# Kernel tuning notes

Measured on AMD Instinct MI355X. Metric: run time of the kernel, lower is better.

The kernel has to match this reference:

```python
import jax, jax.numpy as jnp
import numpy as np

N, E = 50000, 640000
D_IN, D_HID, D_OUT = 128, 128, 64
NEG_SLOPE = 0.2  # PyG SuperGATConv default negative_slope


def setup_inputs() -> dict:
    key = jax.random.key(0)
    ks = jax.random.split(key, 16)
    def glorot(k, shape):
        fan = sum(shape) if len(shape) > 1 else shape[0]
        return jax.random.normal(k, shape, jnp.float32) * np.sqrt(2.0 / fan)
    return {
        "x": jax.random.normal(ks[0], (N, D_IN), jnp.float32),
        "edge_index": jax.random.randint(ks[1], (2, E), 0, N, jnp.int64 if jax.config.jax_enable_x64 else jnp.int32),
        "W0": glorot(ks[2], (D_IN, D_HID)),
        "al0": glorot(ks[3], (D_HID,)),
        "ar0": glorot(ks[4], (D_HID,)),
        "b0": jnp.zeros((D_HID,), jnp.float32),
        "W1": glorot(ks[5], (D_HID, D_HID)),
        "al1": glorot(ks[6], (D_HID,)),
        "ar1": glorot(ks[7], (D_HID,)),
        "b1": jnp.zeros((D_HID,), jnp.float32),
        "W2": glorot(ks[8], (D_HID, D_OUT)),
        "al2": glorot(ks[9], (D_OUT,)),
        "ar2": glorot(ks[10], (D_OUT,)),
        "b2": jnp.zeros((D_OUT,), jnp.float32),
    }


def _supergat_layer(x, W, att_l, att_r, b, src, dst, n):
    # heads = 1, concat=False, attention_type='MX' (PyG SuperGATConv defaults)
    h = x @ W                                   # [N, C]
    hi = h[dst]                                 # target-node features x_i, [Etot, C]
    hj = h[src]                                 # source-node features x_j, [Etot, C]
    logits = jnp.sum(hi * hj, axis=-1)          # MX dot-product gate
    alpha = hj @ att_l + hi @ att_r             # GO-style scores
    alpha = alpha * jax.nn.sigmoid(logits)      # MX mixing
    alpha = jnp.where(alpha >= 0, alpha, NEG_SLOPE * alpha)  # leaky_relu
    # segment softmax over incoming edges of each target node
    amax = jax.ops.segment_max(alpha, dst, num_segments=n)
    ex = jnp.exp(alpha - amax[dst])
    denom = jax.ops.segment_sum(ex, dst, num_segments=n)
    a = ex / (denom[dst] + 1e-16)
    out = jax.ops.segment_sum(hj * a[:, None], dst, num_segments=n)
    return out + b


def reference(x, edge_index, W0, al0, ar0, b0, W1, al1, ar1, b1, W2, al2, ar2, b2):
    n = x.shape[0]
    loops = jnp.arange(n, dtype=edge_index.dtype)  # add_self_loops=True
    src = jnp.concatenate([edge_index[0], loops])
    dst = jnp.concatenate([edge_index[1], loops])
    params = [(W0, al0, ar0, b0), (W1, al1, ar1, b1), (W2, al2, ar2, b2)]
    h = x
    for (W, al, ar, b) in params:
        h = _supergat_layer(h, W, al, ar, b, src, dst, n)
        h = jax.nn.relu(h)          # dropout is identity in eval mode
    return jax.nn.log_softmax(h, axis=-1)
```

## Files before the change

### kernel.cpp

```cpp
#include <hip/hip_runtime.h>
#include <math.h>

using short8 = __attribute__((ext_vector_type(8))) short;
using f32x4 = __attribute__((ext_vector_type(4))) float;

__device__ __forceinline__ float bflo(unsigned int u) {
  union { unsigned int i; float f; } v; v.i = u << 16; return v.f;
}
__device__ __forceinline__ float bfhi(unsigned int u) {
  union { unsigned int i; float f; } v; v.i = u & 0xFFFF0000u; return v.f;
}
__device__ __forceinline__ unsigned short f2bf1(float f) {
  union { float f; unsigned int i; } v; v.f = f;
  return (unsigned short)((v.i + 0x7FFFu + ((v.i >> 16) & 1u)) >> 16);
}
__device__ __forceinline__ unsigned int f2bf_pack(float a, float b) {
  union { float f; unsigned int i; } x, y; x.f = a; y.f = b;
  unsigned int xa = x.i + 0x7FFFu + ((x.i >> 16) & 1u);
  unsigned int yb = y.i + 0x7FFFu + ((y.i >> 16) & 1u);
  return (xa >> 16) | (yb & 0xFFFF0000u);
}

__global__ void prep0_kernel(const float* __restrict__ W0, const float* __restrict__ W1,
                             const float* __restrict__ W2, unsigned short* __restrict__ Wt0,
                             unsigned short* __restrict__ Wt1, unsigned short* __restrict__ Wt2,
                             int* __restrict__ counts, int* __restrict__ dhist, int N) {
  int i = blockIdx.x * 256 + threadIdx.x;
  int gs = gridDim.x * 256;
  for (int j = i; j < N; j += gs) counts[j] = 0;
  if (i < 1024) dhist[i] = 0;
  for (int j = i; j < 128 * 128; j += gs) {
    int c = j >> 7, k = j & 127;
    Wt0[c * 136 + k] = f2bf1(W0[(size_t)k * 128 + c]);
  }
  for (int j = i; j < 128 * 128; j += gs) {
    int c = j >> 7, k = j & 127;
    Wt1[c * 136 + k] = f2bf1(W1[(size_t)k * 128 + c]);
  }
  for (int j = i; j < 64 * 128; j += gs) {
    int c = j >> 7, k = j & 127;
    Wt2[c * 136 + k] = f2bf1(W2[(size_t)k * 64 + c]);
  }
}

__global__ void histo_kernel(const int* __restrict__ ei, int E, int N,
                             int* __restrict__ counts) {
  int e = blockIdx.x * blockDim.x + threadIdx.x;
  int etot = E + N;
  if (e >= etot) return;
  int d = (e < E) ? ei[E + e] : (e - E);
  atomicAdd(&counts[d], 1);
}

__global__ void scan1_deghist_kernel(const int* __restrict__ counts, int* __restrict__ excl,
                                     int* __restrict__ bsums, int* __restrict__ dhist, int N) {
  __shared__ int sm[256];
  __shared__ int lh[1024];
  int t = threadIdx.x;
  int i = blockIdx.x * 256 + t;
  int v = (i < N) ? counts[i] : 0;
  sm[t] = v;
  __syncthreads();
#pragma unroll
  for (int off = 1; off < 256; off <<= 1) {
    int add = (t >= off) ? sm[t - off] : 0;
    __syncthreads();
    sm[t] += add;
    __syncthreads();
  }
  if (i < N) excl[i] = sm[t] - v;
  if (t == 255) bsums[blockIdx.x] = sm[255];
  for (int q = t; q < 1024; q += 256) lh[q] = 0;
  __syncthreads();
  if (i < N) {
    int key = v < 1023 ? v : 1023;
    atomicAdd(&lh[key], 1);
  }
  __syncthreads();
  for (int q = t; q < 1024; q += 256) {
    int c = lh[q];
    if (c) atomicAdd(&dhist[q], c);
  }
}

__global__ void scan2_degscan_kernel(int* __restrict__ bsums, int nb,
                                     int* __restrict__ dhist) {
  int t = threadIdx.x;
  if (blockIdx.x == 0) {
    __shared__ int sm[256];
    int v = (t < nb) ? bsums[t] : 0;
    sm[t] = v;
    __syncthreads();
#pragma unroll
    for (int off = 1; off < 256; off <<= 1) {
      int add = (t >= off) ? sm[t - off] : 0;
      __syncthreads();
      sm[t] += add;
      __syncthreads();
    }
    if (t < nb) bsums[t] = sm[t] - v;
  } else {
    __shared__ int arr[256];
    int v0 = dhist[t * 4 + 0], v1 = dhist[t * 4 + 1];
    int v2 = dhist[t * 4 + 2], v3 = dhist[t * 4 + 3];
    int s0 = v0, s1 = s0 + v1, s2 = s1 + v2, s3 = s2 + v3;
    arr[t] = s3;
    __syncthreads();
#pragma unroll
    for (int off = 1; off < 256; off <<= 1) {
      int add = (t >= off) ? arr[t - off] : 0;
      __syncthreads();
      arr[t] += add;
      __syncthreads();
    }
    int base = (t > 0) ? arr[t - 1] : 0;
    dhist[t * 4 + 0] = base;
    dhist[t * 4 + 1] = base + s0;
    dhist[t * 4 + 2] = base + s1;
    dhist[t * 4 + 3] = base + s2;
  }
}

__global__ void scan3_kernel(const int* __restrict__ excl, const int* __restrict__ bsums,
                             int* __restrict__ rowptr, int* __restrict__ cursor,
                             int N, int etot) {
  int i = blockIdx.x * 256 + threadIdx.x;
  if (i < N) {
    int v = excl[i] + bsums[i >> 8];
    rowptr[i] = v;
    cursor[i] = v;
  }
  if (i == N) rowptr[N] = etot;
}

__global__ void scatter_degscatter_kernel(const int* __restrict__ ei, int E, int N,
                                          int* __restrict__ cursor, int* __restrict__ csr_src,
                                          const int* __restrict__ rowptr,
                                          int* __restrict__ dhist, int* __restrict__ perm) {
  int t = threadIdx.x;
  int e = blockIdx.x * 256 + t;
  int etot = E + N;
  if (e < etot) {
    int s, d;
    if (e < E) { s = ei[e]; d = ei[E + e]; } else { s = e - E; d = e - E; }
    int pos = atomicAdd(&cursor[d], 1);
    csr_src[pos] = s;
  }
  if (blockIdx.x < (N + 255) / 256) {
    __shared__ int lc[1024];
    __shared__ int lb[1024];
    for (int q = t; q < 1024; q += 256) lc[q] = 0;
    __syncthreads();
    int i = blockIdx.x * 256 + t;
    int key = 0, lr = 0;
    if (i < N) {
      int d = rowptr[i + 1] - rowptr[i];
      key = d < 1023 ? d : 1023;
      lr = atomicAdd(&lc[key], 1);
    }
    __syncthreads();
    for (int q = t; q < 1024; q += 256) {
      int c = lc[q];
      if (c) lb[q] = atomicAdd(&dhist[q], c);
    }
    __syncthreads();
    if (i < N) perm[lb[key] + lr] = i;
  }
}

template <int COLS, bool AF32>
__global__ __launch_bounds__(256) void gemm_mfma(
    const void* __restrict__ Xv, const unsigned short* __restrict__ Wt,
    const float* __restrict__ al, const float* __restrict__ ar,
    unsigned short* __restrict__ H, float* __restrict__ hl,
    float* __restrict__ hr, int N) {
  constexpr int NT = COLS / 16;
  __shared__ unsigned short Ws[COLS * 136];
  const int tid = threadIdx.x;
  {
    const unsigned int* wg = (const unsigned int*)Wt;
    unsigned int* ws = (unsigned int*)Ws;
    for (int i = tid; i < COLS * 68; i += 256) ws[i] = wg[i];
  }
  __syncthreads();

  const int w = tid >> 6, l = tid & 63;
  const int l15 = l & 15, lg = l >> 4;
  const int r0 = blockIdx.x * 64 + w * 16;

  f32x4 acc[NT];
#pragma unroll
  for (int t = 0; t < NT; ++t)
#pragma unroll
    for (int j = 0; j < 4; ++j) acc[t][j] = 0.f;

  int arow = r0 + l15;
  if (arow > N - 1) arow = N - 1;

#pragma unroll
  for (int ks = 0; ks < 4; ++ks) {
    short8 af;
    if constexpr (AF32) {
      const float* xp = (const float*)Xv + (size_t)arow * 128 + ks * 32 + lg * 8;
      float4 x0 = *(const float4*)xp;
      float4 x1 = *(const float4*)(xp + 4);
      af[0] = (short)f2bf1(x0.x); af[1] = (short)f2bf1(x0.y);
      af[2] = (short)f2bf1(x0.z); af[3] = (short)f2bf1(x0.w);
      af[4] = (short)f2bf1(x1.x); af[5] = (short)f2bf1(x1.y);
      af[6] = (short)f2bf1(x1.z); af[7] = (short)f2bf1(x1.w);
    } else {
      af = *(const short8*)((const unsigned short*)Xv + (size_t)arow * 128 + ks * 32 + lg * 8);
    }
#pragma unroll
    for (int t = 0; t < NT; ++t) {
      short8 bf = *(const short8*)(&Ws[(t * 16 + l15) * 136 + ks * 32 + lg * 8]);
      acc[t] = __builtin_amdgcn_mfma_f32_16x16x32_bf16(af, bf, acc[t], 0, 0, 0);
    }
  }

  const int orow = r0 + lg * 4;
  float pl4[4] = {0.f, 0.f, 0.f, 0.f}, pr4[4] = {0.f, 0.f, 0.f, 0.f};
#pragma unroll
  for (int t = 0; t < NT; ++t) {
    float av = al[t * 16 + l15], rv = ar[t * 16 + l15];
#pragma unroll
    for (int r = 0; r < 4; ++r) {
      pl4[r] = fmaf(acc[t][r], av, pl4[r]);
      pr4[r] = fmaf(acc[t][r], rv, pr4[r]);
    }
#pragma unroll
    for (int r = 0; r < 4; ++r) {
      int row = orow + r;
      if (row < N) H[(size_t)row * COLS + t * 16 + l15] = f2bf1(acc[t][r]);
    }
  }
#pragma unroll
  for (int off = 1; off < 16; off <<= 1) {
#pragma unroll
    for (int r = 0; r < 4; ++r) {
      pl4[r] += __shfl_xor(pl4[r], off);
      pr4[r] += __shfl_xor(pr4[r], off);
    }
  }
  if (l15 == 0) {
#pragma unroll
    for (int r = 0; r < 4; ++r) {
      int row = orow + r;
      if (row < N) { hl[row] = pl4[r]; hr[row] = pr4[r]; }
    }
  }
}

template <int COLS, bool LAST>
__global__ __launch_bounds__(256, 6) void node_kernel(
    const unsigned short* __restrict__ H, const float* __restrict__ hl,
    const float* __restrict__ hr, const int* __restrict__ rowptr,
    const int* __restrict__ csr_src, const int* __restrict__ perm,
    const float* __restrict__ b, void* __restrict__ OUTv, int N) {
  constexpr int GS = 16;
  constexpr int EPL = COLS / GS;
  constexpr int NU = EPL / 2;
  const int lane = threadIdx.x & 63;
  const int g = lane >> 4, l = lane & 15;
  const int C = (N + 3) / 4;
  const int c = blockIdx.x * 4 + (threadIdx.x >> 6);
  const int idx = g * C + c;
  const bool active = (c < C) && (idx < N);
  const int node = active ? perm[idx] : 0;

  float hi[EPL];
  {
    unsigned int tmp[NU];
    const unsigned short* hp = H + (size_t)node * COLS + l * EPL;
    if constexpr (NU == 4) *(uint4*)tmp = *(const uint4*)hp;
    else                   *(uint2*)tmp = *(const uint2*)hp;
#pragma unroll
    for (int u = 0; u < NU; ++u) { hi[2 * u] = bflo(tmp[u]); hi[2 * u + 1] = bfhi(tmp[u]); }
  }
  const float hri = hr[node];
  const int start = active ? rowptr[node] : 0;
  const int end = active ? rowptr[node + 1] : 0;

  float m = -INFINITY, sumw = 0.f;
  float acc[EPL];
#pragma unroll
  for (int j = 0; j < EPL; ++j) acc[j] = 0.f;

  unsigned int hvA[NU], hvB[NU];
  float hlA = 0.f, hlB = 0.f;
  int e = start;
  if (e < end) {
    int s = csr_src[e];
    hlA = hl[s];
    const unsigned short* hp = H + (size_t)s * COLS + l * EPL;
    if constexpr (NU == 4) *(uint4*)hvA = *(const uint4*)hp;
    else                   *(uint2*)hvA = *(const uint2*)hp;
  }
  if (e + 1 < end) {
    int s = csr_src[e + 1];
    hlB = hl[s];
    const unsigned short* hp = H + (size_t)s * COLS + l * EPL;
    if constexpr (NU == 4) *(uint4*)hvB = *(const uint4*)hp;
    else                   *(uint2*)hvB = *(const uint2*)hp;
  }
  int i2 = (e + 2 < end) ? csr_src[e + 2] : 0;
  int i3 = (e + 3 < end) ? csr_src[e + 3] : 0;

  auto COMPUTE = [&](const float* ch, float chl) {
    float d = 0.f;
#pragma unroll
    for (int j = 0; j < EPL; ++j) d = fmaf(hi[j], ch[j], d);
    d += __shfl_xor(d, 1);
    d += __shfl_xor(d, 2);
    d += __shfl_xor(d, 4);
    d += __shfl_xor(d, 8);
    float gate = 1.f / (1.f + __expf(-d));
    float a = (chl + hri) * gate;
    a = (a >= 0.f) ? a : 0.2f * a;
    float dm = a - m;
    if (dm > 30.f) {
      float sc = __expf(-dm);
      sumw *= sc;
#pragma unroll
      for (int j = 0; j < EPL; ++j) acc[j] *= sc;
      m = a;
      dm = 0.f;
    }
    float w = __expf(dm);
    sumw += w;
#pragma unroll
    for (int j = 0; j < EPL; ++j) acc[j] = fmaf(w, ch[j], acc[j]);
  };

  while (e + 1 < end) {
    float chA[EPL], chB[EPL];
#pragma unroll
    for (int u = 0; u < NU; ++u) { chA[2 * u] = bflo(hvA[u]); chA[2 * u + 1] = bfhi(hvA[u]); }
    float clA = hlA;
    if (e + 2 < end) {
      hlA = hl[i2];
      const unsigned short* hp = H + (size_t)i2 * COLS + l * EPL;
      if constexpr (NU == 4) *(uint4*)hvA = *(const uint4*)hp;
      else                   *(uint2*)hvA = *(const uint2*)hp;
    }
#pragma unroll
    for (int u = 0; u < NU; ++u) { chB[2 * u] = bflo(hvB[u]); chB[2 * u + 1] = bfhi(hvB[u]); }
    float clB = hlB;
    if (e + 3 < end) {
      hlB = hl[i3];
      const unsigned short* hp = H + (size_t)i3 * COLS + l * EPL;
      if constexpr (NU == 4) *(uint4*)hvB = *(const uint4*)hp;
      else                   *(uint2*)hvB = *(const uint2*)hp;
    }
    i2 = (e + 4 < end) ? csr_src[e + 4] : 0;
    i3 = (e + 5 < end) ? csr_src[e + 5] : 0;
    COMPUTE(chA, clA);
    COMPUTE(chB, clB);
    e += 2;
  }
  if (e < end) {
    float chA[EPL];
#pragma unroll
    for (int u = 0; u < NU; ++u) { chA[2 * u] = bflo(hvA[u]); chA[2 * u + 1] = bfhi(hvA[u]); }
    COMPUTE(chA, hlA);
  }

  if (active) {
    const float inv = 1.f / (sumw + 1e-16f);
    float o[EPL];
    const float* bp = b + l * EPL;
#pragma unroll
    for (int j = 0; j < EPL; ++j) o[j] = fmaxf(acc[j] * inv + bp[j], 0.f);

    if constexpr (LAST) {
      float* OUT = (float*)OUTv;
      float mx = o[0];
#pragma unroll
      for (int j = 1; j < EPL; ++j) mx = fmaxf(mx, o[j]);
      mx = fmaxf(mx, __shfl_xor(mx, 1));
      mx = fmaxf(mx, __shfl_xor(mx, 2));
      mx = fmaxf(mx, __shfl_xor(mx, 4));
      mx = fmaxf(mx, __shfl_xor(mx, 8));
      float es = 0.f;
#pragma unroll
      for (int j = 0; j < EPL; ++j) es += __expf(o[j] - mx);
      es += __shfl_xor(es, 1);
      es += __shfl_xor(es, 2);
      es += __shfl_xor(es, 4);
      es += __shfl_xor(es, 8);
      float ls = logf(es);
      float4 ov = make_float4(o[0] - mx - ls, o[1] - mx - ls,
                              o[2] - mx - ls, o[3] - mx - ls);
      *(float4*)(&OUT[(size_t)node * 64 + l * 4]) = ov;
    } else {
      unsigned short* OUT = (unsigned short*)OUTv;
      unsigned int pk[NU];
#pragma unroll
      for (int u = 0; u < NU; ++u) pk[u] = f2bf_pack(o[2 * u], o[2 * u + 1]);
      *(uint4*)(OUT + (size_t)node * COLS + l * EPL) =
          make_uint4(pk[0], pk[1], pk[2], pk[3]);
    }
  }
}

extern "C" void kernel_launch(void* const* d_in, const int* in_sizes, int n_in,
                              void* d_out, int out_size, void* d_ws, size_t ws_size,
                              hipStream_t stream) {
  const float* x = (const float*)d_in[0];
  const int* ei = (const int*)d_in[1];
  const float* W0 = (const float*)d_in[2];
  const float* al0 = (const float*)d_in[3];
  const float* ar0 = (const float*)d_in[4];
  const float* b0 = (const float*)d_in[5];
  const float* W1 = (const float*)d_in[6];
  const float* al1 = (const float*)d_in[7];
  const float* ar1 = (const float*)d_in[8];
  const float* b1 = (const float*)d_in[9];
  const float* W2 = (const float*)d_in[10];
  const float* al2 = (const float*)d_in[11];
  const float* ar2 = (const float*)d_in[12];
  const float* b2 = (const float*)d_in[13];

  const int N = in_sizes[0] / 128;
  const int E = in_sizes[1] / 2;
  const int ETOT = E + N;

  char* p = (char*)d_ws;
  auto carve = [&](size_t bytes) {
    void* r = (void*)p;
    p += (bytes + 255) & ~(size_t)255;
    return r;
  };
  unsigned short* Hb = (unsigned short*)carve((size_t)N * 128 * 2);
  unsigned short* Ob = (unsigned short*)carve((size_t)N * 128 * 2);
  float* hl = (float*)carve((size_t)N * sizeof(float));
  float* hr = (float*)carve((size_t)N * sizeof(float));
  int* counts = (int*)carve((size_t)N * sizeof(int));
  int* excl = (int*)carve((size_t)N * sizeof(int));
  int* bsums = (int*)carve(1024 * sizeof(int));
  int* rowptr = (int*)carve((size_t)(N + 1) * sizeof(int));
  int* cursor = (int*)carve((size_t)(N + 1) * sizeof(int));
  int* csr_src = (int*)carve((size_t)ETOT * sizeof(int));
  int* dhist = (int*)carve(1024 * sizeof(int));
  int* perm = (int*)carve((size_t)N * sizeof(int));
  unsigned short* Wt0 = (unsigned short*)carve(128 * 136 * 2);
  unsigned short* Wt1 = (unsigned short*)carve(128 * 136 * 2);
  unsigned short* Wt2 = (unsigned short*)carve(64 * 136 * 2);

  const int nbs = (N + 255) / 256;
  const int nbe = (ETOT + 255) / 256;

  prep0_kernel<<<nbs, 256, 0, stream>>>(W0, W1, W2, Wt0, Wt1, Wt2, counts, dhist, N);
  histo_kernel<<<nbe, 256, 0, stream>>>(ei, E, N, counts);
  scan1_deghist_kernel<<<nbs, 256, 0, stream>>>(counts, excl, bsums, dhist, N);
  scan2_degscan_kernel<<<2, 256, 0, stream>>>(bsums, nbs, dhist);
  scan3_kernel<<<(N + 256) / 256 + 1, 256, 0, stream>>>(excl, bsums, rowptr, cursor, N, ETOT);
  scatter_degscatter_kernel<<<nbe, 256, 0, stream>>>(ei, E, N, cursor, csr_src, rowptr,
                                                     dhist, perm);

  const int gemm_grid = (N + 63) / 64;
  const int C = (N + 3) / 4;
  const int node_grid = (C + 3) / 4;

  gemm_mfma<128, true><<<gemm_grid, 256, 0, stream>>>(x, Wt0, al0, ar0, Hb, hl, hr, N);
  node_kernel<128, false><<<node_grid, 256, 0, stream>>>(Hb, hl, hr, rowptr, csr_src, perm, b0, Ob, N);

  gemm_mfma<128, false><<<gemm_grid, 256, 0, stream>>>(Ob, Wt1, al1, ar1, Hb, hl, hr, N);
  node_kernel<128, false><<<node_grid, 256, 0, stream>>>(Hb, hl, hr, rowptr, csr_src, perm, b1, Ob, N);

  gemm_mfma<64, false><<<gemm_grid, 256, 0, stream>>>(Ob, Wt2, al2, ar2, Hb, hl, hr, N);
  node_kernel<64, true><<<node_grid, 256, 0, stream>>>(Hb, hl, hr, rowptr, csr_src, perm, b2,
                                                       d_out, N);
}
```

Before: 227.1 us.

## Build CSR with two-level bucketed radix partition instead of global atomics

Replaces the per-node global atomic histogram and atomic scatter with a two-pass bucketed partition. Edges are first grouped into 196 coarse buckets of 256 destination nodes using shared-memory counting and a staged scatter. Each bucket is then sorted locally into CSR within one block. This aims to cut global atomic contention and random scattered writes, at the cost of an extra edge buffer pass and more kernels. NBUCKET is hardcoded to 196, which assumes N <= 50176.

```diff
diff --git a/kernel.cpp b/kernel.cpp
--- a/kernel.cpp
+++ b/kernel.cpp
@@ -21,13 +21,15 @@
   return (xa >> 16) | (yb & 0xFFFF0000u);
 }
 
+#define NBUCKET 196
+
 __global__ void prep0_kernel(const float* __restrict__ W0, const float* __restrict__ W1,
                              const float* __restrict__ W2, unsigned short* __restrict__ Wt0,
                              unsigned short* __restrict__ Wt1, unsigned short* __restrict__ Wt2,
-                             int* __restrict__ counts, int* __restrict__ dhist, int N) {
+                             int* __restrict__ ccnt, int* __restrict__ dhist) {
   int i = blockIdx.x * 256 + threadIdx.x;
   int gs = gridDim.x * 256;
-  for (int j = i; j < N; j += gs) counts[j] = 0;
+  if (i < NBUCKET) ccnt[i] = 0;
   if (i < 1024) dhist[i] = 0;
   for (int j = i; j < 128 * 128; j += gs) {
     int c = j >> 7, k = j & 127;
@@ -43,22 +45,30 @@
   }
 }
 
-__global__ void histo_kernel(const int* __restrict__ ei, int E, int N,
-                             int* __restrict__ counts) {
-  int e = blockIdx.x * blockDim.x + threadIdx.x;
+__global__ __launch_bounds__(1024) void ccount_kernel(const int* __restrict__ ei, int E,
+                                                      int N, int* __restrict__ ccnt) {
+  __shared__ int lc[256];
+  int t = threadIdx.x;
+  if (t < 256) lc[t] = 0;
+  __syncthreads();
+  int e = blockIdx.x * 1024 + t;
   int etot = E + N;
-  if (e >= etot) return;
-  int d = (e < E) ? ei[E + e] : (e - E);
-  atomicAdd(&counts[d], 1);
-}
-
-__global__ void scan1_deghist_kernel(const int* __restrict__ counts, int* __restrict__ excl,
-                                     int* __restrict__ bsums, int* __restrict__ dhist, int N) {
+  if (e < etot) {
+    int d = (e < E) ? ei[E + e] : (e - E);
+    atomicAdd(&lc[d >> 8], 1);
+  }
+  __syncthreads();
+  if (t < NBUCKET) {
+    int c = lc[t];
+    if (c) atomicAdd(&ccnt[t], c);
+  }
+}
+
+__global__ void cscan_kernel(const int* __restrict__ ccnt, int* __restrict__ cbase,
+                             int* __restrict__ gcursor, int etot) {
   __shared__ int sm[256];
-  __shared__ int lh[1024];
   int t = threadIdx.x;
-  int i = blockIdx.x * 256 + t;
-  int v = (i < N) ? counts[i] : 0;
+  int v = (t < NBUCKET) ? ccnt[t] : 0;
   sm[t] = v;
   __syncthreads();
 #pragma unroll
@@ -68,104 +78,162 @@
     sm[t] += add;
     __syncthreads();
   }
-  if (i < N) excl[i] = sm[t] - v;
-  if (t == 255) bsums[blockIdx.x] = sm[255];
-  for (int q = t; q < 1024; q += 256) lh[q] = 0;
-  __syncthreads();
+  if (t < NBUCKET) {
+    int ex = sm[t] - v;
+    cbase[t] = ex;
+    gcursor[t] = ex;
+  }
+  if (t == 0) cbase[NBUCKET] = etot;
+}
+
+__global__ __launch_bounds__(1024) void bscatter_kernel(
+    const int* __restrict__ ei, int E, int N, int* __restrict__ gcursor,
+    uint2* __restrict__ ebuf) {
+  __shared__ int cnt[256], excl[256], base[256];
+  __shared__ uint2 buf[4096];
+  const int t = threadIdx.x;
+  const int etot = E + N;
+  const int e0 = blockIdx.x * 4096;
+  if (t < 256) cnt[t] = 0;
+  __syncthreads();
+
+  int sj[4], dj[4], rj[4], bj[4];
+  bool vj[4];
+#pragma unroll
+  for (int j = 0; j < 4; ++j) {
+    int e = e0 + j * 1024 + t;
+    vj[j] = e < etot;
+    if (vj[j]) {
+      if (e < E) { sj[j] = ei[e]; dj[j] = ei[E + e]; }
+      else       { sj[j] = e - E; dj[j] = e - E; }
+      bj[j] = dj[j] >> 8;
+      rj[j] = atomicAdd(&cnt[bj[j]], 1);
+    }
+  }
+  __syncthreads();
+  if (t < 256) excl[t] = cnt[t];
+  __syncthreads();
+#pragma unroll
+  for (int off = 1; off < 256; off <<= 1) {
+    int add = 0;
+    if (t < 256 && t >= off) add = excl[t - off];
+    __syncthreads();
+    if (t < 256) excl[t] += add;
+    __syncthreads();
+  }
+  if (t < 256) excl[t] -= cnt[t];
+  __syncthreads();
+  if (t < NBUCKET) {
+    int c = cnt[t];
+    base[t] = c ? atomicAdd(&gcursor[t], c) : 0;
+  }
+  __syncthreads();
+#pragma unroll
+  for (int j = 0; j < 4; ++j)
+    if (vj[j]) buf[excl[bj[j]] + rj[j]] = make_uint2((unsigned)sj[j], (unsigned)dj[j]);
+  __syncthreads();
+  int nv = etot - e0;
+  if (nv > 4096) nv = 4096;
+#pragma unroll
+  for (int j = 0; j < 4; ++j) {
+    int i = j * 1024 + t;
+    if (i < nv) {
+      uint2 u = buf[i];
+      int b = (int)(u.y >> 8);
+      ebuf[base[b] + (i - excl[b])] = u;
+    }
+  }
+}
+
+__global__ __launch_bounds__(1024) void bcsr_kernel(
+    const uint2* __restrict__ ebuf, const int* __restrict__ cbase,
+    int* __restrict__ rowptr, int* __restrict__ csr_src, int* __restrict__ dhist,
+    int N, int etot) {
+  __shared__ int hist[256], hexcl[256];
+  const int b = blockIdx.x;
+  const int t = threadIdx.x;
+  const int lo = cbase[b], hi = cbase[b + 1];
+  const int node0 = b * 256;
+  int nn = N - node0;
+  if (nn > 256) nn = 256;
+  if (t < 256) hist[t] = 0;
+  __syncthreads();
+  for (int i = lo + t; i < hi; i += 1024) {
+    int ln = (int)(ebuf[i].y & 255u);
+    atomicAdd(&hist[ln], 1);
+  }
+  __syncthreads();
+  if (t < nn) {
+    int key = hist[t] < 1023 ? hist[t] : 1023;
+    atomicAdd(&dhist[key], 1);
+  }
+  if (t < 256) hexcl[t] = hist[t];
+  __syncthreads();
+#pragma unroll
+  for (int off = 1; off < 256; off <<= 1) {
+    int add = 0;
+    if (t < 256 && t >= off) add = hexcl[t - off];
+    __syncthreads();
+    if (t < 256) hexcl[t] += add;
+    __syncthreads();
+  }
+  if (t < 256) hexcl[t] -= hist[t];
+  __syncthreads();
+  if (t < nn) rowptr[node0 + t] = lo + hexcl[t];
+  if (b == gridDim.x - 1 && t == 0) rowptr[N] = etot;
+  if (t < 256) hist[t] = hexcl[t];
+  __syncthreads();
+  for (int i = lo + t; i < hi; i += 1024) {
+    uint2 u = ebuf[i];
+    int ln = (int)(u.y & 255u);
+    int r = atomicAdd(&hist[ln], 1);
+    csr_src[lo + r] = (int)u.x;
+  }
+}
+
+__global__ void degscan_kernel(int* __restrict__ dhist) {
+  __shared__ int arr[256];
+  int t = threadIdx.x;
+  int v0 = dhist[t * 4 + 0], v1 = dhist[t * 4 + 1];
+  int v2 = dhist[t * 4 + 2], v3 = dhist[t * 4 + 3];
+  int s0 = v0, s1 = s0 + v1, s2 = s1 + v2, s3 = s2 + v3;
+  arr[t] = s3;
+  __syncthreads();
+#pragma unroll
+  for (int off = 1; off < 256; off <<= 1) {
+    int add = (t >= off) ? arr[t - off] : 0;
+    __syncthreads();
+    arr[t] += add;
+    __syncthreads();
+  }
+  int base = (t > 0) ? arr[t - 1] : 0;
+  dhist[t * 4 + 0] = base;
+  dhist[t * 4 + 1] = base + s0;
+  dhist[t * 4 + 2] = base + s1;
+  dhist[t * 4 + 3] = base + s2;
+}
+
+__global__ void degscatter_kernel(const int* __restrict__ rowptr, int N,
+                                  int* __restrict__ dhist, int* __restrict__ perm) {
+  __shared__ int lc[1024];
+  __shared__ int lb[1024];
+  int t = threadIdx.x;
+  for (int i = t; i < 1024; i += 256) lc[i] = 0;
+  __syncthreads();
+  int i = blockIdx.x * 256 + t;
+  int key = 0, lr = 0;
   if (i < N) {
-    int key = v < 1023 ? v : 1023;
-    atomicAdd(&lh[key], 1);
+    int d = rowptr[i + 1] - rowptr[i];
+    key = d < 1023 ? d : 1023;
+    lr = atomicAdd(&lc[key], 1);
   }
   __syncthreads();
   for (int q = t; q < 1024; q += 256) {
-    int c = lh[q];
-    if (c) atomicAdd(&dhist[q], c);
-  }
-}
-
-__global__ void scan2_degscan_kernel(int* __restrict__ bsums, int nb,
-                                     int* __restrict__ dhist) {
-  int t = threadIdx.x;
-  if (blockIdx.x == 0) {
-    __shared__ int sm[256];
-    int v = (t < nb) ? bsums[t] : 0;
-    sm[t] = v;
-    __syncthreads();
-#pragma unroll
-    for (int off = 1; off < 256; off <<= 1) {
-      int add = (t >= off) ? sm[t - off] : 0;
-      __syncthreads();
-      sm[t] += add;
-      __syncthreads();
-    }
-    if (t < nb) bsums[t] = sm[t] - v;
-  } else {
-    __shared__ int arr[256];
-    int v0 = dhist[t * 4 + 0], v1 = dhist[t * 4 + 1];
-    int v2 = dhist[t * 4 + 2], v3 = dhist[t * 4 + 3];
-    int s0 = v0, s1 = s0 + v1, s2 = s1 + v2, s3 = s2 + v3;
-    arr[t] = s3;
-    __syncthreads();
-#pragma unroll
-    for (int off = 1; off < 256; off <<= 1) {
-      int add = (t >= off) ? arr[t - off] : 0;
-      __syncthreads();
-      arr[t] += add;
-      __syncthreads();
-    }
-    int base = (t > 0) ? arr[t - 1] : 0;
-    dhist[t * 4 + 0] = base;
-    dhist[t * 4 + 1] = base + s0;
-    dhist[t * 4 + 2] = base + s1;
-    dhist[t * 4 + 3] = base + s2;
-  }
-}
-
-__global__ void scan3_kernel(const int* __restrict__ excl, const int* __restrict__ bsums,
-                             int* __restrict__ rowptr, int* __restrict__ cursor,
-                             int N, int etot) {
-  int i = blockIdx.x * 256 + threadIdx.x;
-  if (i < N) {
-    int v = excl[i] + bsums[i >> 8];
-    rowptr[i] = v;
-    cursor[i] = v;
-  }
-  if (i == N) rowptr[N] = etot;
-}
-
-__global__ void scatter_degscatter_kernel(const int* __restrict__ ei, int E, int N,
-                                          int* __restrict__ cursor, int* __restrict__ csr_src,
-                                          const int* __restrict__ rowptr,
-                                          int* __restrict__ dhist, int* __restrict__ perm) {
-  int t = threadIdx.x;
-  int e = blockIdx.x * 256 + t;
-  int etot = E + N;
-  if (e < etot) {
-    int s, d;
-    if (e < E) { s = ei[e]; d = ei[E + e]; } else { s = e - E; d = e - E; }
-    int pos = atomicAdd(&cursor[d], 1);
-    csr_src[pos] = s;
-  }
-  if (blockIdx.x < (N + 255) / 256) {
-    __shared__ int lc[1024];
-    __shared__ int lb[1024];
-    for (int q = t; q < 1024; q += 256) lc[q] = 0;
-    __syncthreads();
-    int i = blockIdx.x * 256 + t;
-    int key = 0, lr = 0;
-    if (i < N) {
-      int d = rowptr[i + 1] - rowptr[i];
-      key = d < 1023 ? d : 1023;
-      lr = atomicAdd(&lc[key], 1);
-    }
-    __syncthreads();
-    for (int q = t; q < 1024; q += 256) {
-      int c = lc[q];
-      if (c) lb[q] = atomicAdd(&dhist[q], c);
-    }
-    __syncthreads();
-    if (i < N) perm[lb[key] + lr] = i;
-  }
+    int c = lc[q];
+    if (c) lb[q] = atomicAdd(&dhist[q], c);
+  }
+  __syncthreads();
+  if (i < N) perm[lb[key] + lr] = i;
 }
 
 template <int COLS, bool AF32>
@@ -435,11 +503,11 @@
   unsigned short* Ob = (unsigned short*)carve((size_t)N * 128 * 2);
   float* hl = (float*)carve((size_t)N * sizeof(float));
   float* hr = (float*)carve((size_t)N * sizeof(float));
-  int* counts = (int*)carve((size_t)N * sizeof(int));
-  int* excl = (int*)carve((size_t)N * sizeof(int));
-  int* bsums = (int*)carve(1024 * sizeof(int));
+  int* ccnt = (int*)carve(256 * sizeof(int));
+  int* cbase = (int*)carve(256 * sizeof(int));
+  int* gcursor = (int*)carve(256 * sizeof(int));
+  uint2* ebuf = (uint2*)carve((size_t)ETOT * sizeof(uint2));
   int* rowptr = (int*)carve((size_t)(N + 1) * sizeof(int));
-  int* cursor = (int*)carve((size_t)(N + 1) * sizeof(int));
   int* csr_src = (int*)carve((size_t)ETOT * sizeof(int));
   int* dhist = (int*)carve(1024 * sizeof(int));
   int* perm = (int*)carve((size_t)N * sizeof(int));
@@ -448,15 +516,14 @@
   unsigned short* Wt2 = (unsigned short*)carve(64 * 136 * 2);
 
   const int nbs = (N + 255) / 256;
-  const int nbe = (ETOT + 255) / 256;
-
-  prep0_kernel<<<nbs, 256, 0, stream>>>(W0, W1, W2, Wt0, Wt1, Wt2, counts, dhist, N);
-  histo_kernel<<<nbe, 256, 0, stream>>>(ei, E, N, counts);
-  scan1_deghist_kernel<<<nbs, 256, 0, stream>>>(counts, excl, bsums, dhist, N);
-  scan2_degscan_kernel<<<2, 256, 0, stream>>>(bsums, nbs, dhist);
-  scan3_kernel<<<(N + 256) / 256 + 1, 256, 0, stream>>>(excl, bsums, rowptr, cursor, N, ETOT);
-  scatter_degscatter_kernel<<<nbe, 256, 0, stream>>>(ei, E, N, cursor, csr_src, rowptr,
-                                                     dhist, perm);
+
+  prep0_kernel<<<nbs, 256, 0, stream>>>(W0, W1, W2, Wt0, Wt1, Wt2, ccnt, dhist);
+  ccount_kernel<<<(ETOT + 1023) / 1024, 1024, 0, stream>>>(ei, E, N, ccnt);
+  cscan_kernel<<<1, 256, 0, stream>>>(ccnt, cbase, gcursor, ETOT);
+  bscatter_kernel<<<(ETOT + 4095) / 4096, 1024, 0, stream>>>(ei, E, N, gcursor, ebuf);
+  bcsr_kernel<<<NBUCKET, 1024, 0, stream>>>(ebuf, cbase, rowptr, csr_src, dhist, N, ETOT);
+  degscan_kernel<<<1, 256, 0, stream>>>(dhist);
+  degscatter_kernel<<<nbs, 256, 0, stream>>>(rowptr, N, dhist, perm);
 
   const int gemm_grid = (N + 63) / 64;
   const int C = (N + 3) / 4;
```

After: 340.2 us. 49.8% more time.
